# Optimization experiments

Hardware: AMD Instinct MI355X
Metric: run time of the kernel (lower is better)

## Reference

```python
import jax, jax.numpy as jnp
import numpy as np
from jax import lax

NUM_CLASSES = 80
STRIDES = (8, 16, 32)
CENTER_RADIUS = 2.5
CANDIDATE_K = 10


def setup_inputs() -> dict:
    key = jax.random.key(0)
    ks = jax.random.split(key, 6)
    B, G, NGT = 32, 50, 20
    out0 = jax.random.normal(ks[0], (B, 85, 80, 80), jnp.float32)
    out1 = jax.random.normal(ks[1], (B, 85, 40, 40), jnp.float32)
    out2 = jax.random.normal(ks[2], (B, 85, 20, 20), jnp.float32)
    cls = jax.random.randint(ks[3], (B, G, 1), 0, NUM_CLASSES).astype(jnp.float32)
    cxcy = jax.random.uniform(ks[4], (B, G, 2), minval=32.0, maxval=608.0)
    wh = jax.random.uniform(ks[5], (B, G, 2), minval=16.0, maxval=128.0)
    labels = jnp.concatenate([cls, cxcy, wh], -1)
    valid = (jnp.arange(G) < NGT)[None, :, None]
    labels = labels * valid  # padded rows are all-zero, as the torch code expects
    return {"out0": out0, "out1": out1, "out2": out2, "labels": labels}


def _decode(out, stride):
    # out: [B, 85, H, W] -> [B, H*W, 85] with xy=(pred+grid)*stride, wh=exp(pred)*stride
    B, C, H, W = out.shape
    o = out.transpose(0, 2, 3, 1).reshape(B, H * W, C)
    yv, xv = jnp.meshgrid(jnp.arange(H), jnp.arange(W), indexing="ij")
    grid = jnp.stack([xv, yv], -1).reshape(H * W, 2).astype(out.dtype)
    xy = (o[..., :2] + grid) * stride
    wh = jnp.exp(o[..., 2:4]) * stride
    dec = jnp.concatenate([xy, wh, o[..., 4:]], -1)
    centers = (grid + 0.5) * stride
    strides = jnp.full((H * W,), float(stride), out.dtype)
    return dec, centers, strides


def _pairwise_iou(a, b):
    # a: [G,4] cxcywh, b: [A,4] cxcywh -> [G,A]
    tl = jnp.maximum(a[:, None, :2] - a[:, None, 2:] * 0.5, b[None, :, :2] - b[None, :, 2:] * 0.5)
    br = jnp.minimum(a[:, None, :2] + a[:, None, 2:] * 0.5, b[None, :, :2] + b[None, :, 2:] * 0.5)
    en = jnp.all(tl < br, -1).astype(a.dtype)
    inter = jnp.prod(br - tl, -1) * en
    area_a = a[:, 2] * a[:, 3]
    area_b = b[:, 2] * b[:, 3]
    return inter / (area_a[:, None] + area_b[None, :] - inter + 1e-12)


def _iou_loss(pred, tgt):
    # elementwise IoU loss (YOLOX IOUloss, loss_type='iou'): 1 - iou^2
    tl = jnp.maximum(pred[..., :2] - pred[..., 2:] * 0.5, tgt[..., :2] - tgt[..., 2:] * 0.5)
    br = jnp.minimum(pred[..., :2] + pred[..., 2:] * 0.5, tgt[..., :2] + tgt[..., 2:] * 0.5)
    en = jnp.all(tl < br, -1).astype(pred.dtype)
    inter = jnp.prod(jnp.clip(br - tl, 0.0), -1) * en
    union = pred[..., 2] * pred[..., 3] + tgt[..., 2] * tgt[..., 3] - inter + 1e-16
    iou = inter / union
    return 1.0 - iou * iou


def _bce_logits(x, y):
    return jnp.maximum(x, 0.0) - x * y + jnp.log1p(jnp.exp(-jnp.abs(x)))


def _assign(boxes, cls_logits, obj_logit, labels_b, centers, strides):
    # Per-image SimOTA. boxes [A,4], cls_logits [A,C], obj_logit [A], labels_b [G,5]
    G = labels_b.shape[0]
    gt_valid = labels_b.sum(-1) > 0                       # [G]
    gt_box = labels_b[:, 1:5]                             # [G,4] cxcywh
    gt_cls = labels_b[:, 0].astype(jnp.int32)
    cx, cy = centers[:, 0], centers[:, 1]
    # in-box test (strict, as min(delta)>0 in torch)
    in_box = ((cx[None] > gt_box[:, 0:1] - 0.5 * gt_box[:, 2:3])
              & (cx[None] < gt_box[:, 0:1] + 0.5 * gt_box[:, 2:3])
              & (cy[None] > gt_box[:, 1:2] - 0.5 * gt_box[:, 3:4])
              & (cy[None] < gt_box[:, 1:2] + 0.5 * gt_box[:, 3:4]))  # [G,A]
    rs = CENTER_RADIUS * strides[None]
    in_ctr = ((jnp.abs(cx[None] - gt_box[:, 0:1]) < rs)
              & (jnp.abs(cy[None] - gt_box[:, 1:2]) < rs))           # [G,A]
    fg = jnp.any((in_box | in_ctr) & gt_valid[:, None], axis=0)       # [A]
    geom = in_box & in_ctr                                            # is_in_boxes_and_center
    cand = fg[None, :] & gt_valid[:, None]                            # valid (gt, anchor) pairs

    iou = _pairwise_iou(gt_box, boxes)                                # [G,A]
    iou_m = jnp.where(cand, iou, 0.0)
    iou_cost = -jnp.log(iou + 1e-8)

    # cls cost without materializing [G,A,C]: p = sqrt(sig(cls)*sig(obj));
    # BCE(p, onehot(g)).sum(C) = -log p[g] + log(1-p[g]) - sum_c log(1-p[c])
    p = jnp.sqrt(jax.nn.sigmoid(cls_logits) * jax.nn.sigmoid(obj_logit)[:, None])  # [A,C]
    p = jnp.clip(p, 1e-7, 1.0 - 1e-6)
    logp = jnp.log(p)
    log1mp = jnp.log1p(-p)
    s = log1mp.sum(-1)                                                # [A]
    lp_g = jnp.take(logp, gt_cls, axis=1).T                           # [G,A]
    l1_g = jnp.take(log1mp, gt_cls, axis=1).T                         # [G,A]
    cls_cost = -lp_g + l1_g - s[None, :]

    cost = (cls_cost + 3.0 * iou_cost
            + 100000.0 * (~geom).astype(cost_dtype := boxes.dtype)
            + 1e9 * (~cand).astype(boxes.dtype))

    # dynamic-k: k_g = clamp(int(sum(topk10 ious)), 1)
    topk_ious = lax.top_k(iou_m, CANDIDATE_K)[0]                      # [G,10]
    dyn_k = jnp.clip(topk_ious.sum(-1).astype(jnp.int32), 1, None)    # [G]
    sorted_cost = jnp.sort(cost, axis=1)
    thr = jnp.take_along_axis(sorted_cost, (dyn_k - 1)[:, None], axis=1)
    match = (cost <= thr) & cand                                      # [G,A]

    # resolve anchors matched to multiple gts: keep global argmin-cost gt
    count = match.sum(0)                                              # [A]
    best_gt = jnp.argmin(cost, axis=0)                                # [A]
    keep = jnp.arange(G)[:, None] == best_gt[None, :]
    match = jnp.where(count[None, :] > 1, match & keep, match)

    fg_final = match.any(0)                                           # [A]
    matched_gt = jnp.argmax(match, axis=0)                            # [A]
    pred_iou = (match.astype(iou.dtype) * iou).sum(0)                 # [A]
    return fg_final, matched_gt, pred_iou, gt_valid


def _forward(out0, out1, out2, labels):
    decs, ctrs, strs = [], [], []
    for o, s in zip((out0, out1, out2), STRIDES):
        d, c, st = _decode(o, s)
        decs.append(d); ctrs.append(c); strs.append(st)
    outputs = jnp.concatenate(decs, axis=1)          # [B, A, 85]
    centers = jnp.concatenate(ctrs, axis=0)          # [A, 2]
    strides = jnp.concatenate(strs, axis=0)          # [A]

    bbox = outputs[..., :4]
    obj = outputs[..., 4]
    cls = outputs[..., 5:]

    assign = jax.vmap(_assign, in_axes=(0, 0, 0, 0, None, None))
    fg, mgt, piou, gt_valid = assign(
        lax.stop_gradient(bbox), lax.stop_gradient(cls),
        lax.stop_gradient(obj), lax.stop_gradient(labels), centers, strides)
    piou = lax.stop_gradient(piou)

    gt_box = lax.stop_gradient(labels[:, :, 1:5])
    reg_t = jnp.take_along_axis(gt_box, mgt[..., None], axis=1)       # [B,A,4]
    gt_cls = labels[..., 0].astype(jnp.int32)
    mcls = jnp.take_along_axis(gt_cls, mgt, axis=1)                   # [B,A]
    cls_t = jax.nn.one_hot(mcls, NUM_CLASSES, dtype=outputs.dtype) * piou[..., None]

    fgf = fg.astype(outputs.dtype)
    num_fg = jnp.maximum(fgf.sum(), 1.0)
    loss_iou = (_iou_loss(bbox, reg_t) * fgf).sum() / num_fg
    loss_obj = _bce_logits(obj, fgf).sum() / num_fg
    loss_cls = (_bce_logits(cls, cls_t).sum(-1) * fgf).sum() / num_fg
    return 5.0 * loss_iou + loss_obj + loss_cls


def reference(out0, out1, out2, labels):
    return _forward(out0, out1, out2, labels)
```

## Files before the change

### kernel.cpp

```cpp
#include <hip/hip_runtime.h>
#include <math.h>

#define B_  32
#define A_  8400
#define G_  50
#define NC_ 80
#define PAD 4352
#define CHK_A 33
#define CHK_C 17
#define NBLK_C (8*4*CHK_C)
#define CLIPHI ((float)(1.0 - 1e-6))

#define ACC_NUMFG 0
#define ACC_IOU   32
#define ACC_OBJ0  64
#define ACC_OBJFG 96
#define ACC_CLS   128

struct AInfo { int lvl; int within; int w; int hw; float s; int x; int y; };

__device__ __forceinline__ AInfo anchor_info(int a) {
  AInfo r;
  if (a < 6400)      { r.lvl = 0; r.within = a;        r.w = 80; r.hw = 6400; r.s = 8.0f;  }
  else if (a < 8000) { r.lvl = 1; r.within = a - 6400; r.w = 40; r.hw = 1600; r.s = 16.0f; }
  else               { r.lvl = 2; r.within = a - 8000; r.w = 20; r.hw = 400;  r.s = 32.0f; }
  r.x = r.within % r.w; r.y = r.within / r.w;
  return r;
}

__device__ __forceinline__ const float* lvl_base(const float* o0, const float* o1,
                                                 const float* o2, int lvl) {
  return lvl == 0 ? o0 : (lvl == 1 ? o1 : o2);
}

__device__ __forceinline__ float2 cost_iou(
    float gx, float gy, float gw, float gh,
    float fx, float fy, float st,
    float4 bx, float ssum, float sobj, float clsv)
{
  float cx = (fx + 0.5f) * st;
  float cy = (fy + 0.5f) * st;
  bool in_box = (cx > gx - 0.5f*gw) && (cx < gx + 0.5f*gw) &&
                (cy > gy - 0.5f*gh) && (cy < gy + 0.5f*gh);
  float rs = 2.5f * st;
  bool in_ctr = (fabsf(cx - gx) < rs) && (fabsf(cy - gy) < rs);
  bool geom = in_box && in_ctr;
  float tlx = fmaxf(gx - gw*0.5f, bx.x - bx.z*0.5f);
  float tly = fmaxf(gy - gh*0.5f, bx.y - bx.w*0.5f);
  float brx = fminf(gx + gw*0.5f, bx.x + bx.z*0.5f);
  float bry = fminf(gy + gh*0.5f, bx.y + bx.w*0.5f);
  bool en = (tlx < brx) && (tly < bry);
  float inter = en ? (brx - tlx) * (bry - tly) : 0.0f;
  float iou = inter / (gw*gh + bx.z*bx.w - inter + 1e-12f);
  float iou_cost = -__logf(iou + 1e-8f);
  float sc = 1.0f / (1.0f + __expf(-clsv));
  float p = sqrtf(sc * sobj);
  p = fminf(fmaxf(p, 1e-7f), CLIPHI);
  float cls_cost = -__logf(p) + __logf(1.0f - p) - ssum;
  float cost = cls_cost + 3.0f * iou_cost;
  if (!geom) cost += 100000.0f;
  return make_float2(cost, iou);
}

__global__ __launch_bounds__(256)
void kA(const float* __restrict__ o0, const float* __restrict__ o1,
        const float* __restrict__ o2, const float* __restrict__ labels,
        float4* __restrict__ cBox, float4* __restrict__ cPack,
        int* __restrict__ ncandP, float* __restrict__ accP)
{
  __shared__ float gl[G_], gr[G_], gtt[G_], gbb[G_], gcx[G_], gcy[G_];
  __shared__ int nvgS;
  __shared__ float wsum[4];
  __shared__ int wcnt[4], wbase[4];
  int j = blockIdx.x;
  int x8 = j & 7, r = j >> 3;
  int b = x8 + 8*(r & 3);
  int chunk = r >> 2;
  int tid = threadIdx.x;
  if (tid < 64) {
    bool v = false; float l0=0,gx=0,gy=0,gw=0,gh=0;
    if (tid < G_) {
      const float* L = labels + (size_t)b*G_*5 + tid*5;
      l0=L[0]; gx=L[1]; gy=L[2]; gw=L[3]; gh=L[4];
      v = (l0+gx+gy+gw+gh) > 0.0f;
    }
    unsigned long long mm = __ballot(v);
    if (tid == 0) nvgS = __popcll(mm);
    if (v) {
      int pos = __popcll(mm & ((1ull << tid) - 1ull));
      gl[pos]  = gx - 0.5f*gw; gr[pos]  = gx + 0.5f*gw;
      gtt[pos] = gy - 0.5f*gh; gbb[pos] = gy + 0.5f*gh;
      gcx[pos] = gx; gcy[pos] = gy;
    }
  }
  __syncthreads();
  int nvg = nvgS;
  int a = chunk*256 + tid;
  float objbce = 0.0f, v4 = 0.0f, so = 0.0f, ss = 0.0f;
  float4 bx = make_float4(0.f,0.f,0.f,0.f);
  bool anyfg = false;
  AInfo ai; const float* base = nullptr;
  if (a < A_) {
    ai = anchor_info(a);
    base = lvl_base(o0,o1,o2,ai.lvl) + (size_t)b*85*ai.hw + ai.within;
    float v0 = base[0];
    float v1 = base[(size_t)1*ai.hw];
    float v2 = base[(size_t)2*ai.hw];
    float v3 = base[(size_t)3*ai.hw];
    v4 = base[(size_t)4*ai.hw];
    bx.x = (v0 + (float)ai.x) * ai.s;
    bx.y = (v1 + (float)ai.y) * ai.s;
    bx.z = __expf(v2) * ai.s;
    bx.w = __expf(v3) * ai.s;
    objbce = fmaxf(v4, 0.0f) + __logf(1.0f + __expf(-fabsf(v4)));
    float cx = ((float)ai.x + 0.5f) * ai.s;
    float cy = ((float)ai.y + 0.5f) * ai.s;
    float rs = 2.5f * ai.s;
    for (int k = 0; k < nvg; k++) {
      bool in_box = (cx > gl[k]) && (cx < gr[k]) && (cy > gtt[k]) && (cy < gbb[k]);
      bool in_ctr = (fabsf(cx - gcx[k]) < rs) && (fabsf(cy - gcy[k]) < rs);
      if (in_box || in_ctr) { anyfg = true; break; }
    }
    so = 1.0f / (1.0f + __expf(-v4));
  }
  if (anyfg) {
    const float* q = base + (size_t)5*ai.hw;
    float s0=0,s1=0,s2=0,s3=0,s4=0,s5=0,s6=0,s7=0;
    for (int c = 0; c < NC_; c += 8) {
      float x0 = q[(size_t)(c+0)*ai.hw];
      float x1 = q[(size_t)(c+1)*ai.hw];
      float x2 = q[(size_t)(c+2)*ai.hw];
      float x3 = q[(size_t)(c+3)*ai.hw];
      float x4 = q[(size_t)(c+4)*ai.hw];
      float x5 = q[(size_t)(c+5)*ai.hw];
      float x6 = q[(size_t)(c+6)*ai.hw];
      float x7 = q[(size_t)(c+7)*ai.hw];
      #define TERM(xx, ss_) { \
        float sc = 1.0f/(1.0f+__expf(-(xx))); \
        float p = sqrtf(sc*so); \
        p = fminf(fmaxf(p,1e-7f), CLIPHI); \
        ss_ += __logf(1.0f - p); }
      TERM(x0,s0) TERM(x1,s1) TERM(x2,s2) TERM(x3,s3)
      TERM(x4,s4) TERM(x5,s5) TERM(x6,s6) TERM(x7,s7)
      #undef TERM
    }
    ss = ((s0+s1)+(s2+s3)) + ((s4+s5)+(s6+s7));
  }
  float v = objbce;
  for (int o = 32; o > 0; o >>= 1) v += __shfl_down(v, o, 64);
  int lane = tid & 63, w = tid >> 6;
  if (lane == 0) wsum[w] = v;
  unsigned long long mm = __ballot(anyfg);
  if (lane == 0) wcnt[w] = __popcll(mm);
  __syncthreads();
  if (tid == 0) {
    atomicAdd(&accP[ACC_OBJ0], wsum[0]+wsum[1]+wsum[2]+wsum[3]);
    int t0=wcnt[0], t1=wcnt[1], t2=wcnt[2], t3=wcnt[3];
    int tot = t0+t1+t2+t3;
    int bas = tot ? atomicAdd(&ncandP[b*64], tot) : 0;
    wbase[0]=bas; wbase[1]=bas+t0; wbase[2]=bas+t0+t1; wbase[3]=bas+t0+t1+t2;
  }
  __syncthreads();
  if (anyfg) {
    int pos = wbase[w] + __popcll(mm & ((1ull << lane) - 1ull));
    if (pos < PAD) {
      cBox[b*PAD + pos]  = bx;
      cPack[b*PAD + pos] = make_float4(ss, so, __int_as_float(a), v4);
    }
  }
}

__global__ __launch_bounds__(256)
void kB(const float* __restrict__ o0, const float* __restrict__ o1,
        const float* __restrict__ o2, const float* __restrict__ labels,
        const float4* __restrict__ cBox, const float4* __restrict__ cPack,
        const int* __restrict__ ncandP, float* __restrict__ thrw,
        float* __restrict__ costM)
{
  __shared__ float sh[256*10];
  __shared__ int s_dk;
  int j = blockIdx.x;
  int x8 = j & 7, r = j >> 3;
  int b = x8 + 8*(r & 3);
  int g = r >> 2;
  int tid = threadIdx.x;
  const float* L = labels + (size_t)(b*G_ + g)*5;
  float l0=L[0], gx=L[1], gy=L[2], gw=L[3], gh=L[4];
  bool gvalid = (l0+gx+gy+gw+gh) > 0.0f;
  if (!gvalid) { if (tid==0) thrw[b*G_+g] = -3.0e38f; return; }
  int gcls = (int)l0;
  int nc = ncandP[b*64]; if (nc > PAD) nc = PAD;
  float* row = costM + ((size_t)b*G_ + g)*(size_t)PAD;
  float ti[10], tc[10];
  #pragma unroll
  for (int jq=0;jq<10;jq++){ ti[jq]=0.0f; tc[jq]=3e38f; }
  for (int i = tid; i < nc; i += 256) {
    float4 bx = cBox[b*PAD + i];
    float4 pk = cPack[b*PAD + i];
    int a = __float_as_int(pk.z);
    AInfo ai = anchor_info(a);
    float clsv = lvl_base(o0,o1,o2,ai.lvl)[(size_t)(b*85 + 5 + gcls)*ai.hw + ai.within];
    float2 ci = cost_iou(gx,gy,gw,gh,(float)ai.x,(float)ai.y,ai.s,
                         bx, pk.x, pk.y, clsv);
    row[i] = ci.x;
    float v = ci.y;
    if (v > ti[9]) {
      #pragma unroll
      for (int jq=0;jq<10;jq++){ float o=ti[jq]; bool t=v>o; ti[jq]=t?v:o; v=t?o:v; }
    }
    float c = ci.x;
    if (c < tc[9]) {
      #pragma unroll
      for (int jq=0;jq<10;jq++){ float o=tc[jq]; bool t=c<o; tc[jq]=t?c:o; c=t?o:c; }
    }
  }
  #pragma unroll
  for (int jq=0;jq<10;jq++) sh[tid*10+jq] = ti[jq];
  __syncthreads();
  for (int str=128; str>0; str>>=1) {
    if (tid < str) {
      float out[10]; int i=0, jj=0;
      float* Aa = &sh[tid*10]; float* Bb = &sh[(tid+str)*10];
      #pragma unroll
      for (int k=0;k<10;k++){ float va=Aa[i], vb=Bb[jj]; bool t=(va>=vb); out[k]=t?va:vb; if(t)i++; else jj++; }
      #pragma unroll
      for (int k=0;k<10;k++) Aa[k]=out[k];
    }
    __syncthreads();
  }
  if (tid==0) {
    float s10=0.0f;
    #pragma unroll
    for (int jq=0;jq<10;jq++) s10 += sh[jq];
    int dk = (int)s10; if (dk<1) dk=1; if (dk>10) dk=10;
    s_dk = dk;
  }
  __syncthreads();
  #pragma unroll
  for (int jq=0;jq<10;jq++) sh[tid*10+jq] = tc[jq];
  __syncthreads();
  for (int str=128; str>0; str>>=1) {
    if (tid < str) {
      float out[10]; int i=0, jj=0;
      float* Aa = &sh[tid*10]; float* Bb = &sh[(tid+str)*10];
      #pragma unroll
      for (int k=0;k<10;k++){ float va=Aa[i], vb=Bb[jj]; bool t=(va<=vb); out[k]=t?va:vb; if(t)i++; else jj++; }
      #pragma unroll
      for (int k=0;k<10;k++) Aa[k]=out[k];
    }
    __syncthreads();
  }
  if (tid==0) thrw[b*G_+g] = sh[s_dk-1];
}

__global__ __launch_bounds__(256)
void kC(const float* __restrict__ o0, const float* __restrict__ o1,
        const float* __restrict__ o2, const float* __restrict__ labels,
        const float4* __restrict__ cBox, const float4* __restrict__ cPack,
        const int* __restrict__ ncandP, const float* __restrict__ thrw,
        const float* __restrict__ costM, float* __restrict__ accP,
        int* __restrict__ doneP, float* __restrict__ out)
{
  __shared__ float labS[G_*5];
  __shared__ float thrS[G_];
  __shared__ int vgIdx[G_];
  __shared__ int nvgS;
  __shared__ float wpart[4][4];
  int j = blockIdx.x;
  int x8 = j & 7, r = j >> 3;
  int b = x8 + 8*(r & 3);
  int chunk = r >> 2;
  int tid = threadIdx.x;
  int nc = ncandP[b*64]; if (nc > PAD) nc = PAD;
  bool active = (chunk*256 < nc);
  if (active) {
    for (int i = tid; i < G_*5; i += 256) labS[i] = labels[(size_t)b*G_*5 + i];
    if (tid < G_) thrS[tid] = thrw[b*G_ + tid];
    __syncthreads();
    if (tid < 64) {
      bool v = false;
      if (tid < G_) {
        float s5 = labS[tid*5]+labS[tid*5+1]+labS[tid*5+2]+labS[tid*5+3]+labS[tid*5+4];
        v = (s5 > 0.0f);
      }
      unsigned long long mm = __ballot(v);
      if (tid == 0) nvgS = __popcll(mm);
      if (v) vgIdx[__popcll(mm & ((1ull << tid) - 1ull))] = tid;
    }
    __syncthreads();
    int nvg = nvgS;
    int i = chunk*256 + tid;
    float accPf=0.f, accIou=0.f, accObjx=0.f, accCls=0.f;
    if (i < nc) {
      const float* cm = costM + (size_t)b*G_*(size_t)PAD + i;
      float minc = 3e38f; int ming = 0;
      int cnt = 0; int firstg = -1;
      for (int k = 0; k < nvg; k++) {
        int g = vgIdx[k];
        float c = cm[(size_t)g*PAD];
        if (c < minc) { minc = c; ming = g; }
        if (c <= thrS[g]) { cnt++; if (firstg < 0) firstg = g; }
      }
      int mg = -1;
      if (cnt == 1)     mg = firstg;
      else if (cnt > 1) { if (minc <= thrS[ming]) mg = ming; }
      if (mg >= 0) {
        float4 bx = cBox[b*PAD + i];
        float4 pk = cPack[b*PAD + i];
        accPf = 1.0f;
        accObjx = pk.w;
        float tx=labS[mg*5+1], ty=labS[mg*5+2], tw=labS[mg*5+3], th=labS[mg*5+4];
        float tlx = fmaxf(tx - tw*0.5f, bx.x - bx.z*0.5f);
        float tly = fmaxf(ty - th*0.5f, bx.y - bx.w*0.5f);
        float brx = fminf(tx + tw*0.5f, bx.x + bx.z*0.5f);
        float bry = fminf(ty + th*0.5f, bx.y + bx.w*0.5f);
        bool en = (tlx < brx) && (tly < bry);
        float inter_p = en ? (brx - tlx) * (bry - tly) : 0.0f;
        float pi = inter_p / (tw*th + bx.z*bx.w - inter_p + 1e-12f);
        float iw = fmaxf(brx-tlx, 0.0f), ih = fmaxf(bry-tly, 0.0f);
        float inter = iw*ih * (en ? 1.0f : 0.0f);
        float uni = bx.z*bx.w + tw*th - inter + 1e-16f;
        float iou2 = inter/uni;
        accIou = 1.0f - iou2*iou2;
        int mcls = (int)labS[mg*5];
        int a = __float_as_int(pk.z);
        AInfo ai = anchor_info(a);
        const float* clsbase = lvl_base(o0,o1,o2,ai.lvl) + (size_t)(b*85 + 5)*ai.hw + ai.within;
        #pragma unroll 4
        for (int c = 0; c < NC_; c++) {
          float x = clsbase[(size_t)c * ai.hw];
          accCls += fmaxf(x,0.0f) - x*((c==mcls)?pi:0.0f) + __logf(1.0f + __expf(-fabsf(x)));
        }
      }
    }
    for (int o = 32; o > 0; o >>= 1) {
      accPf   += __shfl_down(accPf,   o, 64);
      accIou  += __shfl_down(accIou,  o, 64);
      accObjx += __shfl_down(accObjx, o, 64);
      accCls  += __shfl_down(accCls,  o, 64);
    }
    int lane = tid & 63, w = tid >> 6;
    if (lane == 0) { wpart[w][0]=accPf; wpart[w][1]=accIou; wpart[w][2]=accObjx; wpart[w][3]=accCls; }
    __syncthreads();
    if (tid == 0) {
      float s0=0.f,s1=0.f,s2=0.f,s3=0.f;
      for (int q=0;q<4;q++){ s0+=wpart[q][0]; s1+=wpart[q][1]; s2+=wpart[q][2]; s3+=wpart[q][3]; }
      if (s0!=0.f) atomicAdd(&accP[ACC_NUMFG], s0);
      if (s1!=0.f) atomicAdd(&accP[ACC_IOU],   s1);
      if (s2!=0.f) atomicAdd(&accP[ACC_OBJFG], s2);
      if (s3!=0.f) atomicAdd(&accP[ACC_CLS],   s3);
    }
  }
  if (tid == 0) {
    __threadfence();
    int old = atomicAdd(doneP, 1);
    if (old == NBLK_C - 1) {
      float nfg  = atomicAdd(&accP[ACC_NUMFG], 0.0f);
      float liou = atomicAdd(&accP[ACC_IOU],   0.0f);
      float obj0 = atomicAdd(&accP[ACC_OBJ0],  0.0f);
      float objf = atomicAdd(&accP[ACC_OBJFG], 0.0f);
      float lcls = atomicAdd(&accP[ACC_CLS],   0.0f);
      float nf = fmaxf(nfg, 1.0f);
      out[0] = (5.0f*liou + (obj0 - objf) + lcls) / nf;
    }
  }
}

extern "C" void kernel_launch(void* const* d_in, const int* in_sizes, int n_in,
                              void* d_out, int out_size, void* d_ws, size_t ws_size,
                              hipStream_t stream)
{
  const float* o0 = (const float*)d_in[0];
  const float* o1 = (const float*)d_in[1];
  const float* o2 = (const float*)d_in[2];
  const float* labels = (const float*)d_in[3];
  char* w = (char*)d_ws;
  size_t off = 0;
  auto alloc = [&](size_t bytes) -> void* {
    void* p = w + off; off += (bytes + 255) & ~(size_t)255; return p;
  };
  char*  ctrl  = (char*)alloc(8192 + 1024 + 256);
  int*   ncandP= (int*)ctrl;
  float* accP  = (float*)(ctrl + 8192);
  int*   doneP = (int*)(ctrl + 8192 + 1024);
  float4* cBox  = (float4*)alloc(sizeof(float4)*(size_t)B_*PAD);
  float4* cPack = (float4*)alloc(sizeof(float4)*(size_t)B_*PAD);
  float*  thrw  = (float*) alloc(sizeof(float)*(size_t)B_*G_);
  float*  costM = (float*) alloc(sizeof(float)*(size_t)B_*G_*(size_t)PAD);

  hipMemsetAsync(ctrl, 0, 8192 + 1024 + 256, stream);

  kA<<<8*4*CHK_A, 256, 0, stream>>>(o0,o1,o2,labels,cBox,cPack,ncandP,accP);
  kB<<<8*4*G_,    256, 0, stream>>>(o0,o1,o2,labels,cBox,cPack,ncandP,thrw,costM);
  kC<<<NBLK_C,    256, 0, stream>>>(o0,o1,o2,labels,cBox,cPack,ncandP,thrw,costM,accP,doneP,(float*)d_out);
}
```

Before: 195.2 us.

## Fuse memset and three kernels into one cooperative persistent kernel

Replaces the memset plus three separate kernel launches with a single cooperative kernel. It uses grid-wide syncs between the candidate-gathering, class-sum, per-GT top-k/threshold and final assignment/loss phases, and grid-stride loops over the work items. The aim is to remove launch gaps and the separate finalize/done-counter logic. In exchange the grid is capped at occupancy×256 blocks and pays for several grid.sync barriers. The old multi-kernel path stays as a fallback if the cooperative launch fails.

Result: slower. 619.6 us (+217.3%).

```diff
diff --git a/kernel.cpp b/kernel.cpp
--- a/kernel.cpp
+++ b/kernel.cpp
@@ -1,5 +1,8 @@
 #include <hip/hip_runtime.h>
+#include <hip/hip_cooperative_groups.h>
 #include <math.h>
+
+namespace cg = cooperative_groups;
 
 #define B_  32
 #define A_  8400
@@ -60,6 +63,315 @@
   float cost = cls_cost + 3.0f * iou_cost;
   if (!geom) cost += 100000.0f;
   return make_float2(cost, iou);
+}
+
+__global__ __launch_bounds__(256)
+void fusedK(const float* __restrict__ o0, const float* __restrict__ o1,
+            const float* __restrict__ o2, const float* __restrict__ labels,
+            float4* __restrict__ cBox, float4* __restrict__ cPack,
+            int* __restrict__ ncandP, float* __restrict__ accP,
+            float* __restrict__ thrw, float* __restrict__ costM,
+            float* __restrict__ out)
+{
+  cg::grid_group grid = cg::this_grid();
+  __shared__ union {
+    struct { float gl[G_], gr[G_], gtt[G_], gbb[G_], gcx[G_], gcy[G_]; } p1;
+    struct { float sh[256*10]; } p3;
+    struct { float labS[G_*5]; float thrS[G_]; int vgIdx[G_]; } p4;
+  } U;
+  __shared__ int nvgS;
+  __shared__ float wred[4];
+  __shared__ int wcnt[4], wbase[4];
+  __shared__ int s_dk;
+  __shared__ float wpart[4][4];
+  int tid = threadIdx.x;
+
+  if (blockIdx.x == 0) {
+    for (int i = tid; i < B_*64; i += 256) ncandP[i] = 0;
+    if (tid < 256) accP[tid] = 0.0f;
+  }
+  grid.sync();
+
+  for (int t = blockIdx.x; t < B_*CHK_A; t += gridDim.x) {
+    __syncthreads();
+    int b = (t & 7) + 8 * ((t >> 3) & 3);
+    int chunk = t >> 5;
+    if (tid < 64) {
+      bool v = false; float l0=0,gx=0,gy=0,gw=0,gh=0;
+      if (tid < G_) {
+        const float* L = labels + (size_t)b*G_*5 + tid*5;
+        l0=L[0]; gx=L[1]; gy=L[2]; gw=L[3]; gh=L[4];
+        v = (l0+gx+gy+gw+gh) > 0.0f;
+      }
+      unsigned long long mm = __ballot(v);
+      if (tid == 0) nvgS = __popcll(mm);
+      if (v) {
+        int pos = __popcll(mm & ((1ull << tid) - 1ull));
+        U.p1.gl[pos]  = gx - 0.5f*gw; U.p1.gr[pos]  = gx + 0.5f*gw;
+        U.p1.gtt[pos] = gy - 0.5f*gh; U.p1.gbb[pos] = gy + 0.5f*gh;
+        U.p1.gcx[pos] = gx; U.p1.gcy[pos] = gy;
+      }
+    }
+    __syncthreads();
+    int nvg = nvgS;
+    int a = chunk*256 + tid;
+    float objbce = 0.0f, v4 = 0.0f, so = 0.0f;
+    float4 bx = make_float4(0.f,0.f,0.f,0.f);
+    bool anyfg = false;
+    if (a < A_) {
+      AInfo ai = anchor_info(a);
+      const float* base = lvl_base(o0,o1,o2,ai.lvl) + (size_t)b*85*ai.hw + ai.within;
+      float v0 = base[0];
+      float v1 = base[(size_t)1*ai.hw];
+      float v2 = base[(size_t)2*ai.hw];
+      float v3 = base[(size_t)3*ai.hw];
+      v4 = base[(size_t)4*ai.hw];
+      bx.x = (v0 + (float)ai.x) * ai.s;
+      bx.y = (v1 + (float)ai.y) * ai.s;
+      bx.z = __expf(v2) * ai.s;
+      bx.w = __expf(v3) * ai.s;
+      objbce = fmaxf(v4, 0.0f) + __logf(1.0f + __expf(-fabsf(v4)));
+      float cx = ((float)ai.x + 0.5f) * ai.s;
+      float cy = ((float)ai.y + 0.5f) * ai.s;
+      float rs = 2.5f * ai.s;
+      for (int k = 0; k < nvg; k++) {
+        bool in_box = (cx > U.p1.gl[k]) && (cx < U.p1.gr[k]) &&
+                      (cy > U.p1.gtt[k]) && (cy < U.p1.gbb[k]);
+        bool in_ctr = (fabsf(cx - U.p1.gcx[k]) < rs) && (fabsf(cy - U.p1.gcy[k]) < rs);
+        if (in_box || in_ctr) { anyfg = true; break; }
+      }
+      so = 1.0f / (1.0f + __expf(-v4));
+    }
+    float v = objbce;
+    for (int o = 32; o > 0; o >>= 1) v += __shfl_down(v, o, 64);
+    int lane = tid & 63, w = tid >> 6;
+    if (lane == 0) wred[w] = v;
+    unsigned long long mm = __ballot(anyfg);
+    if (lane == 0) wcnt[w] = __popcll(mm);
+    __syncthreads();
+    if (tid == 0) {
+      atomicAdd(&accP[ACC_OBJ0], wred[0]+wred[1]+wred[2]+wred[3]);
+      int t0=wcnt[0], t1=wcnt[1], t2=wcnt[2], t3=wcnt[3];
+      int tot = t0+t1+t2+t3;
+      int bas = tot ? atomicAdd(&ncandP[b*64], tot) : 0;
+      wbase[0]=bas; wbase[1]=bas+t0; wbase[2]=bas+t0+t1; wbase[3]=bas+t0+t1+t2;
+    }
+    __syncthreads();
+    if (anyfg) {
+      int pos = wbase[w] + __popcll(mm & ((1ull << lane) - 1ull));
+      if (pos < PAD) {
+        cBox[b*PAD + pos]  = bx;
+        cPack[b*PAD + pos] = make_float4(0.0f, so, __int_as_float(a), v4);
+      }
+    }
+  }
+  grid.sync();
+
+  for (int t = blockIdx.x; t < B_*CHK_C; t += gridDim.x) {
+    int b = (t & 7) + 8 * ((t >> 3) & 3);
+    int chunk = t >> 5;
+    int nc = ncandP[b*64]; if (nc > PAD) nc = PAD;
+    int i = chunk*256 + tid;
+    if (i >= nc) continue;
+    float4 pk = cPack[b*PAD + i];
+    float so = pk.y;
+    int a = __float_as_int(pk.z);
+    AInfo ai = anchor_info(a);
+    const float* q = lvl_base(o0,o1,o2,ai.lvl) + (size_t)(b*85 + 5)*ai.hw + ai.within;
+    float s0=0,s1=0,s2=0,s3=0,s4=0,s5=0,s6=0,s7=0;
+    for (int c = 0; c < NC_; c += 8) {
+      float x0 = q[(size_t)(c+0)*ai.hw];
+      float x1 = q[(size_t)(c+1)*ai.hw];
+      float x2 = q[(size_t)(c+2)*ai.hw];
+      float x3 = q[(size_t)(c+3)*ai.hw];
+      float x4 = q[(size_t)(c+4)*ai.hw];
+      float x5 = q[(size_t)(c+5)*ai.hw];
+      float x6 = q[(size_t)(c+6)*ai.hw];
+      float x7 = q[(size_t)(c+7)*ai.hw];
+      #define TERM(xx, ss_) { \
+        float sc = 1.0f/(1.0f+__expf(-(xx))); \
+        float p = sqrtf(sc*so); \
+        p = fminf(fmaxf(p,1e-7f), CLIPHI); \
+        ss_ += __logf(1.0f - p); }
+      TERM(x0,s0) TERM(x1,s1) TERM(x2,s2) TERM(x3,s3)
+      TERM(x4,s4) TERM(x5,s5) TERM(x6,s6) TERM(x7,s7)
+      #undef TERM
+    }
+    float ss = ((s0+s1)+(s2+s3)) + ((s4+s5)+(s6+s7));
+    ((float*)&cPack[b*PAD + i])[0] = ss;
+  }
+  grid.sync();
+
+  for (int t = blockIdx.x; t < B_*G_; t += gridDim.x) {
+    __syncthreads();
+    int b = (t & 7) + 8 * ((t >> 3) & 3);
+    int g = t >> 5;
+    const float* L = labels + (size_t)(b*G_ + g)*5;
+    float l0=L[0], gx=L[1], gy=L[2], gw=L[3], gh=L[4];
+    bool gvalid = (l0+gx+gy+gw+gh) > 0.0f;
+    if (!gvalid) { if (tid==0) thrw[b*G_+g] = -3.0e38f; continue; }
+    int gcls = (int)l0;
+    int nc = ncandP[b*64]; if (nc > PAD) nc = PAD;
+    float* row = costM + ((size_t)b*G_ + g)*(size_t)PAD;
+    float ti[10], tc[10];
+    #pragma unroll
+    for (int jq=0;jq<10;jq++){ ti[jq]=0.0f; tc[jq]=3e38f; }
+    for (int i = tid; i < nc; i += 256) {
+      float4 bx = cBox[b*PAD + i];
+      float4 pk = cPack[b*PAD + i];
+      int a = __float_as_int(pk.z);
+      AInfo ai = anchor_info(a);
+      float clsv = lvl_base(o0,o1,o2,ai.lvl)[(size_t)(b*85 + 5 + gcls)*ai.hw + ai.within];
+      float2 ci = cost_iou(gx,gy,gw,gh,(float)ai.x,(float)ai.y,ai.s,
+                           bx, pk.x, pk.y, clsv);
+      row[i] = ci.x;
+      float v = ci.y;
+      if (v > ti[9]) {
+        #pragma unroll
+        for (int jq=0;jq<10;jq++){ float o=ti[jq]; bool tt=v>o; ti[jq]=tt?v:o; v=tt?o:v; }
+      }
+      float c = ci.x;
+      if (c < tc[9]) {
+        #pragma unroll
+        for (int jq=0;jq<10;jq++){ float o=tc[jq]; bool tt=c<o; tc[jq]=tt?c:o; c=tt?o:c; }
+      }
+    }
+    #pragma unroll
+    for (int jq=0;jq<10;jq++) U.p3.sh[tid*10+jq] = ti[jq];
+    __syncthreads();
+    for (int str=128; str>0; str>>=1) {
+      if (tid < str) {
+        float outv[10]; int i=0, jj=0;
+        float* Aa = &U.p3.sh[tid*10]; float* Bb = &U.p3.sh[(tid+str)*10];
+        #pragma unroll
+        for (int k=0;k<10;k++){ float va=Aa[i], vb=Bb[jj]; bool tt=(va>=vb); outv[k]=tt?va:vb; if(tt)i++; else jj++; }
+        #pragma unroll
+        for (int k=0;k<10;k++) Aa[k]=outv[k];
+      }
+      __syncthreads();
+    }
+    if (tid==0) {
+      float s10=0.0f;
+      #pragma unroll
+      for (int jq=0;jq<10;jq++) s10 += U.p3.sh[jq];
+      int dk = (int)s10; if (dk<1) dk=1; if (dk>10) dk=10;
+      s_dk = dk;
+    }
+    __syncthreads();
+    #pragma unroll
+    for (int jq=0;jq<10;jq++) U.p3.sh[tid*10+jq] = tc[jq];
+    __syncthreads();
+    for (int str=128; str>0; str>>=1) {
+      if (tid < str) {
+        float outv[10]; int i=0, jj=0;
+        float* Aa = &U.p3.sh[tid*10]; float* Bb = &U.p3.sh[(tid+str)*10];
+        #pragma unroll
+        for (int k=0;k<10;k++){ float va=Aa[i], vb=Bb[jj]; bool tt=(va<=vb); outv[k]=tt?va:vb; if(tt)i++; else jj++; }
+        #pragma unroll
+        for (int k=0;k<10;k++) Aa[k]=outv[k];
+      }
+      __syncthreads();
+    }
+    if (tid==0) thrw[b*G_+g] = U.p3.sh[s_dk-1];
+  }
+  grid.sync();
+
+  for (int t = blockIdx.x; t < B_*CHK_C; t += gridDim.x) {
+    __syncthreads();
+    int b = (t & 7) + 8 * ((t >> 3) & 3);
+    int chunk = t >> 5;
+    int nc = ncandP[b*64]; if (nc > PAD) nc = PAD;
+    if (chunk*256 >= nc) continue;
+    for (int i = tid; i < G_*5; i += 256) U.p4.labS[i] = labels[(size_t)b*G_*5 + i];
+    if (tid < G_) U.p4.thrS[tid] = thrw[b*G_ + tid];
+    __syncthreads();
+    if (tid < 64) {
+      bool v = false;
+      if (tid < G_) {
+        float s5 = U.p4.labS[tid*5]+U.p4.labS[tid*5+1]+U.p4.labS[tid*5+2]
+                 + U.p4.labS[tid*5+3]+U.p4.labS[tid*5+4];
+        v = (s5 > 0.0f);
+      }
+      unsigned long long mm = __ballot(v);
+      if (tid == 0) nvgS = __popcll(mm);
+      if (v) U.p4.vgIdx[__popcll(mm & ((1ull << tid) - 1ull))] = tid;
+    }
+    __syncthreads();
+    int nvg = nvgS;
+    int i = chunk*256 + tid;
+    float accPf=0.f, accIou=0.f, accObjx=0.f, accCls=0.f;
+    if (i < nc) {
+      const float* cm = costM + (size_t)b*G_*(size_t)PAD + i;
+      float minc = 3e38f; int ming = 0;
+      int cnt = 0; int firstg = -1;
+      for (int k = 0; k < nvg; k++) {
+        int g = U.p4.vgIdx[k];
+        float c = cm[(size_t)g*PAD];
+        if (c < minc) { minc = c; ming = g; }
+        if (c <= U.p4.thrS[g]) { cnt++; if (firstg < 0) firstg = g; }
+      }
+      int mg = -1;
+      if (cnt == 1)     mg = firstg;
+      else if (cnt > 1) { if (minc <= U.p4.thrS[ming]) mg = ming; }
+      if (mg >= 0) {
+        float4 bx = cBox[b*PAD + i];
+        float4 pk = cPack[b*PAD + i];
+        accPf = 1.0f;
+        accObjx = pk.w;
+        float tx=U.p4.labS[mg*5+1], ty=U.p4.labS[mg*5+2];
+        float tw=U.p4.labS[mg*5+3], th=U.p4.labS[mg*5+4];
+        float tlx = fmaxf(tx - tw*0.5f, bx.x - bx.z*0.5f);
+        float tly = fmaxf(ty - th*0.5f, bx.y - bx.w*0.5f);
+        float brx = fminf(tx + tw*0.5f, bx.x + bx.z*0.5f);
+        float bry = fminf(ty + th*0.5f, bx.y + bx.w*0.5f);
+        bool en = (tlx < brx) && (tly < bry);
+        float inter_p = en ? (brx - tlx) * (bry - tly) : 0.0f;
+        float pi = inter_p / (tw*th + bx.z*bx.w - inter_p + 1e-12f);
+        float iw = fmaxf(brx-tlx, 0.0f), ih = fmaxf(bry-tly, 0.0f);
+        float inter = iw*ih * (en ? 1.0f : 0.0f);
+        float uni = bx.z*bx.w + tw*th - inter + 1e-16f;
+        float iou2 = inter/uni;
+        accIou = 1.0f - iou2*iou2;
+        int mcls = (int)U.p4.labS[mg*5];
+        int a = __float_as_int(pk.z);
+        AInfo ai = anchor_info(a);
+        const float* clsbase = lvl_base(o0,o1,o2,ai.lvl) + (size_t)(b*85 + 5)*ai.hw + ai.within;
+        #pragma unroll 4
+        for (int c = 0; c < NC_; c++) {
+          float x = clsbase[(size_t)c * ai.hw];
+          accCls += fmaxf(x,0.0f) - x*((c==mcls)?pi:0.0f) + __logf(1.0f + __expf(-fabsf(x)));
+        }
+      }
+    }
+    for (int o = 32; o > 0; o >>= 1) {
+      accPf   += __shfl_down(accPf,   o, 64);
+      accIou  += __shfl_down(accIou,  o, 64);
+      accObjx += __shfl_down(accObjx, o, 64);
+      accCls  += __shfl_down(accCls,  o, 64);
+    }
+    int lane = tid & 63, w = tid >> 6;
+    if (lane == 0) { wpart[w][0]=accPf; wpart[w][1]=accIou; wpart[w][2]=accObjx; wpart[w][3]=accCls; }
+    __syncthreads();
+    if (tid == 0) {
+      float s0=0.f,s1=0.f,s2=0.f,s3=0.f;
+      for (int q=0;q<4;q++){ s0+=wpart[q][0]; s1+=wpart[q][1]; s2+=wpart[q][2]; s3+=wpart[q][3]; }
+      if (s0!=0.f) atomicAdd(&accP[ACC_NUMFG], s0);
+      if (s1!=0.f) atomicAdd(&accP[ACC_IOU],   s1);
+      if (s2!=0.f) atomicAdd(&accP[ACC_OBJFG], s2);
+      if (s3!=0.f) atomicAdd(&accP[ACC_CLS],   s3);
+    }
+  }
+  grid.sync();
+
+  if (blockIdx.x == 0 && tid == 0) {
+    float nfg  = atomicAdd(&accP[ACC_NUMFG], 0.0f);
+    float liou = atomicAdd(&accP[ACC_IOU],   0.0f);
+    float obj0 = atomicAdd(&accP[ACC_OBJ0],  0.0f);
+    float objf = atomicAdd(&accP[ACC_OBJFG], 0.0f);
+    float lcls = atomicAdd(&accP[ACC_CLS],   0.0f);
+    float nf = fmaxf(nfg, 1.0f);
+    out[0] = (5.0f*liou + (obj0 - objf) + lcls) / nf;
+  }
 }
 
 __global__ __launch_bounds__(256)
@@ -387,10 +699,24 @@
   float4* cPack = (float4*)alloc(sizeof(float4)*(size_t)B_*PAD);
   float*  thrw  = (float*) alloc(sizeof(float)*(size_t)B_*G_);
   float*  costM = (float*) alloc(sizeof(float)*(size_t)B_*G_*(size_t)PAD);
+  float*  outp  = (float*)d_out;
+
+  int occ = 0;
+  hipError_t oe = hipOccupancyMaxActiveBlocksPerMultiprocessor(&occ, fusedK, 256, 0);
+  bool coop_ok = (oe == hipSuccess) && (occ >= 1);
+  if (coop_ok) {
+    int grid = occ * 256;
+    if (grid > 1024) grid = 1024;
+    void* args[] = { (void*)&o0, (void*)&o1, (void*)&o2, (void*)&labels,
+                     (void*)&cBox, (void*)&cPack, (void*)&ncandP, (void*)&accP,
+                     (void*)&thrw, (void*)&costM, (void*)&outp };
+    hipError_t le = hipLaunchCooperativeKernel((void*)fusedK, dim3(grid), dim3(256),
+                                               args, 0, stream);
+    if (le == hipSuccess) return;
+  }
 
   hipMemsetAsync(ctrl, 0, 8192 + 1024 + 256, stream);
-
   kA<<<8*4*CHK_A, 256, 0, stream>>>(o0,o1,o2,labels,cBox,cPack,ncandP,accP);
   kB<<<8*4*G_,    256, 0, stream>>>(o0,o1,o2,labels,cBox,cPack,ncandP,thrw,costM);
-  kC<<<NBLK_C,    256, 0, stream>>>(o0,o1,o2,labels,cBox,cPack,ncandP,thrw,costM,accP,doneP,(float*)d_out);
+  kC<<<NBLK_C,    256, 0, stream>>>(o0,o1,o2,labels,cBox,cPack,ncandP,thrw,costM,accP,doneP,outp);
 }
```

## Compact divergent per-anchor class loops into dense work lists in kA and kC

Applied to the files above, without the earlier changes.

In kA, the candidate anchors of each block are first compacted into shared-memory lists, and the 80-class cost-sum loop then runs over that dense list. Before, only the threads with anyfg did the loop, which left warps divergent. In kC, matched anchors are likewise compacted, and the class BCE is computed cooperatively, with one wavefront per anchor and lanes spread across classes. This turns strided per-thread reads into coalesced-ish parallel work. The cost is extra shared memory, more syncs and an extra atomic per wave. The order of floating-point summation also changes.

Measured after the change: 184.6 us. -5.5%, faster.

```diff
diff --git a/kernel.cpp b/kernel.cpp
--- a/kernel.cpp
+++ b/kernel.cpp
@@ -72,6 +72,8 @@
   __shared__ int nvgS;
   __shared__ float wsum[4];
   __shared__ int wcnt[4], wbase[4];
+  __shared__ int aL[256];
+  __shared__ float soL[256], v4L[256];
   int j = blockIdx.x;
   int x8 = j & 7, r = j >> 3;
   int b = x8 + 8*(r & 3);
@@ -96,13 +98,12 @@
   __syncthreads();
   int nvg = nvgS;
   int a = chunk*256 + tid;
-  float objbce = 0.0f, v4 = 0.0f, so = 0.0f, ss = 0.0f;
+  float objbce = 0.0f, v4 = 0.0f, so = 0.0f;
   float4 bx = make_float4(0.f,0.f,0.f,0.f);
   bool anyfg = false;
-  AInfo ai; const float* base = nullptr;
   if (a < A_) {
-    ai = anchor_info(a);
-    base = lvl_base(o0,o1,o2,ai.lvl) + (size_t)b*85*ai.hw + ai.within;
+    AInfo ai = anchor_info(a);
+    const float* base = lvl_base(o0,o1,o2,ai.lvl) + (size_t)b*85*ai.hw + ai.within;
     float v0 = base[0];
     float v1 = base[(size_t)1*ai.hw];
     float v2 = base[(size_t)2*ai.hw];
@@ -123,8 +124,37 @@
     }
     so = 1.0f / (1.0f + __expf(-v4));
   }
+  float v = objbce;
+  for (int o = 32; o > 0; o >>= 1) v += __shfl_down(v, o, 64);
+  int lane = tid & 63, w = tid >> 6;
+  if (lane == 0) wsum[w] = v;
+  unsigned long long mm = __ballot(anyfg);
+  if (lane == 0) wcnt[w] = __popcll(mm);
+  __syncthreads();
+  if (tid == 0) {
+    atomicAdd(&accP[ACC_OBJ0], wsum[0]+wsum[1]+wsum[2]+wsum[3]);
+    int t0=wcnt[0], t1=wcnt[1], t2=wcnt[2], t3=wcnt[3];
+    int tot = t0+t1+t2+t3;
+    int bas = tot ? atomicAdd(&ncandP[b*64], tot) : 0;
+    wbase[0]=bas; wbase[1]=bas+t0; wbase[2]=bas+t0+t1; wbase[3]=bas+t0+t1+t2;
+  }
+  __syncthreads();
   if (anyfg) {
-    const float* q = base + (size_t)5*ai.hw;
+    int pre = __popcll(mm & ((1ull << lane) - 1ull));
+    int lpos = (wbase[w] - wbase[0]) + pre;
+    aL[lpos] = a; soL[lpos] = so; v4L[lpos] = v4;
+    int pos = wbase[w] + pre;
+    if (pos < PAD) cBox[b*PAD + pos] = bx;
+  }
+  __syncthreads();
+  int base0 = wbase[0];
+  int tot = (wbase[3] + wcnt[3]) - base0;
+  for (int t = tid; t < tot; t += 256) {
+    if (base0 + t >= PAD) break;
+    int a2 = aL[t];
+    float so2 = soL[t];
+    AInfo ai = anchor_info(a2);
+    const float* q = lvl_base(o0,o1,o2,ai.lvl) + (size_t)(b*85 + 5)*ai.hw + ai.within;
     float s0=0,s1=0,s2=0,s3=0,s4=0,s5=0,s6=0,s7=0;
     for (int c = 0; c < NC_; c += 8) {
       float x0 = q[(size_t)(c+0)*ai.hw];
@@ -137,36 +167,15 @@
       float x7 = q[(size_t)(c+7)*ai.hw];
       #define TERM(xx, ss_) { \
         float sc = 1.0f/(1.0f+__expf(-(xx))); \
-        float p = sqrtf(sc*so); \
+        float p = sqrtf(sc*so2); \
         p = fminf(fmaxf(p,1e-7f), CLIPHI); \
         ss_ += __logf(1.0f - p); }
       TERM(x0,s0) TERM(x1,s1) TERM(x2,s2) TERM(x3,s3)
       TERM(x4,s4) TERM(x5,s5) TERM(x6,s6) TERM(x7,s7)
       #undef TERM
     }
-    ss = ((s0+s1)+(s2+s3)) + ((s4+s5)+(s6+s7));
-  }
-  float v = objbce;
-  for (int o = 32; o > 0; o >>= 1) v += __shfl_down(v, o, 64);
-  int lane = tid & 63, w = tid >> 6;
-  if (lane == 0) wsum[w] = v;
-  unsigned long long mm = __ballot(anyfg);
-  if (lane == 0) wcnt[w] = __popcll(mm);
-  __syncthreads();
-  if (tid == 0) {
-    atomicAdd(&accP[ACC_OBJ0], wsum[0]+wsum[1]+wsum[2]+wsum[3]);
-    int t0=wcnt[0], t1=wcnt[1], t2=wcnt[2], t3=wcnt[3];
-    int tot = t0+t1+t2+t3;
-    int bas = tot ? atomicAdd(&ncandP[b*64], tot) : 0;
-    wbase[0]=bas; wbase[1]=bas+t0; wbase[2]=bas+t0+t1; wbase[3]=bas+t0+t1+t2;
-  }
-  __syncthreads();
-  if (anyfg) {
-    int pos = wbase[w] + __popcll(mm & ((1ull << lane) - 1ull));
-    if (pos < PAD) {
-      cBox[b*PAD + pos]  = bx;
-      cPack[b*PAD + pos] = make_float4(ss, so, __int_as_float(a), v4);
-    }
+    float ss = ((s0+s1)+(s2+s3)) + ((s4+s5)+(s6+s7));
+    cPack[b*PAD + base0 + t] = make_float4(ss, so2, __int_as_float(a2), v4L[t]);
   }
 }
 
@@ -266,6 +275,10 @@
   __shared__ int vgIdx[G_];
   __shared__ int nvgS;
   __shared__ float wpart[4][4];
+  __shared__ int aML[256];
+  __shared__ float piML[256];
+  __shared__ int mclsML[256];
+  __shared__ int mcntS;
   int j = blockIdx.x;
   int x8 = j & 7, r = j >> 3;
   int b = x8 + 8*(r & 3);
@@ -276,6 +289,7 @@
   if (active) {
     for (int i = tid; i < G_*5; i += 256) labS[i] = labels[(size_t)b*G_*5 + i];
     if (tid < G_) thrS[tid] = thrw[b*G_ + tid];
+    if (tid == 0) mcntS = 0;
     __syncthreads();
     if (tid < 64) {
       bool v = false;
@@ -291,6 +305,7 @@
     int nvg = nvgS;
     int i = chunk*256 + tid;
     float accPf=0.f, accIou=0.f, accObjx=0.f, accCls=0.f;
+    bool matched = false; int m_a = 0; float m_pi = 0.0f; int m_cls = 0;
     if (i < nc) {
       const float* cm = costM + (size_t)b*G_*(size_t)PAD + i;
       float minc = 3e38f; int ming = 0;
@@ -322,14 +337,38 @@
         float uni = bx.z*bx.w + tw*th - inter + 1e-16f;
         float iou2 = inter/uni;
         accIou = 1.0f - iou2*iou2;
-        int mcls = (int)labS[mg*5];
-        int a = __float_as_int(pk.z);
-        AInfo ai = anchor_info(a);
+        matched = true;
+        m_a = __float_as_int(pk.z);
+        m_pi = pi;
+        m_cls = (int)labS[mg*5];
+      }
+    }
+    {
+      int lane = tid & 63;
+      unsigned long long mm = __ballot(matched);
+      int cnt = __popcll(mm);
+      int bpos = 0;
+      if (lane == 0 && cnt) bpos = atomicAdd(&mcntS, cnt);
+      bpos = __shfl(bpos, 0, 64);
+      if (matched) {
+        int p = bpos + __popcll(mm & ((1ull << lane) - 1ull));
+        aML[p] = m_a; piML[p] = m_pi; mclsML[p] = m_cls;
+      }
+    }
+    __syncthreads();
+    {
+      int lane = tid & 63, w = tid >> 6;
+      int mcount = mcntS;
+      for (int idx = w; idx < mcount; idx += 4) {
+        int a2 = aML[idx]; float pi2 = piML[idx]; int mc = mclsML[idx];
+        AInfo ai = anchor_info(a2);
         const float* clsbase = lvl_base(o0,o1,o2,ai.lvl) + (size_t)(b*85 + 5)*ai.hw + ai.within;
-        #pragma unroll 4
-        for (int c = 0; c < NC_; c++) {
-          float x = clsbase[(size_t)c * ai.hw];
-          accCls += fmaxf(x,0.0f) - x*((c==mcls)?pi:0.0f) + __logf(1.0f + __expf(-fabsf(x)));
+        float x1 = clsbase[(size_t)lane * ai.hw];
+        accCls += fmaxf(x1,0.0f) - x1*((lane==mc)?pi2:0.0f) + __logf(1.0f + __expf(-fabsf(x1)));
+        if (lane < NC_ - 64) {
+          int c2 = lane + 64;
+          float x2 = clsbase[(size_t)c2 * ai.hw];
+          accCls += fmaxf(x2,0.0f) - x2*((c2==mc)?pi2:0.0f) + __logf(1.0f + __expf(-fabsf(x2)));
         }
       }
     }
```
